# Kernel tuning notes

Hardware: AMD Instinct MI355X
Metric: run time of the kernel (lower is better)

## Reference

```python
import jax, jax.numpy as jnp
import numpy as np

B, T, N, F = 4, 24, 10000, 64
E = 160000
K_STEPS = 3
HID = 128


def setup_inputs() -> dict:
    key = jax.random.key(0)
    ks = jax.random.split(key, 12)
    history = jax.random.normal(ks[0], (B, T, N, F), dtype=jnp.float32)
    horizon = jax.random.normal(ks[1], (B, 6, N, F), dtype=jnp.float32)
    edge_index = jax.random.randint(ks[2], (2, E), 0, N, dtype=jnp.int64)
    s = 1.0 / np.sqrt(F)
    W_enc = jax.random.normal(ks[3], (F, F), dtype=jnp.float32) * s
    W_hor = jax.random.normal(ks[4], (F, F), dtype=jnp.float32) * s
    b_enc = jnp.zeros((F,), dtype=jnp.float32)
    W_fc = jax.random.normal(ks[5], (F, F), dtype=jnp.float32) * s  # EventGAN.fc (no bias)
    b_gcn = jax.random.normal(ks[6], (F,), dtype=jnp.float32) * 0.01  # EventGAN.bias
    W1 = jax.random.normal(ks[7], (T * F, HID), dtype=jnp.float32) / np.sqrt(T * F)
    b1 = jnp.zeros((HID,), dtype=jnp.float32)
    W2 = jax.random.normal(ks[8], (HID, 1), dtype=jnp.float32) / np.sqrt(HID)
    b2 = jnp.zeros((1,), dtype=jnp.float32)
    return {"history": history, "horizon": horizon, "edge_index": edge_index,
            "W_enc": W_enc, "W_hor": W_hor, "b_enc": b_enc,
            "W_fc": W_fc, "b_gcn": b_gcn,
            "W1": W1, "b1": b1, "W2": W2, "b2": b2}


def _event_gan_step(h, row, col, norm, W_fc, b_gcn, n_nodes):
    # h: [B, N, F]; GCN-style normalized sum aggregation (EventGAN.forward)
    x = h @ W_fc  # fc, no bias
    msgs = norm[None, :, None] * x[:, row, :]  # [B, Etot, F] gather + scale
    agg = jax.vmap(lambda m: jax.ops.segment_sum(m, col, num_segments=n_nodes))(msgs)
    return agg + b_gcn


def reference(history, horizon, edge_index, W_enc, W_hor, b_enc, W_fc, b_gcn, W1, b1, W2, b2):
    b, t, n, f = history.shape
    # FeatureEncoder (stand-in): per-timestep linear over F mixing pooled horizon context
    hor_ctx = jnp.mean(horizon, axis=1) @ W_hor  # [B, N, F]
    x = jnp.tanh(jnp.einsum('btnf,fg->btng', history, W_enc) + hor_ctx[:, None, :, :] + b_enc)
    # spatial: k-step EventGAN propagation on last timestep's exogenous features
    h = x[:, -1, :, -f:]  # [B, N, F] (F == exogenous_features)
    row0, col0 = edge_index[0], edge_index[1]
    loops = jnp.arange(n, dtype=edge_index.dtype)
    row = jnp.concatenate([row0, loops])
    col = jnp.concatenate([col0, loops])
    deg = jax.ops.segment_sum(jnp.ones_like(col, dtype=h.dtype), col, num_segments=n)
    dinv = jnp.where(deg > 0, jax.lax.rsqrt(jnp.maximum(deg, 1.0)), 0.0)
    norm = dinv[row] * dinv[col]
    for _ in range(K_STEPS):
        h = _event_gan_step(h, row, col, norm, W_fc, b_gcn, n)
    x = x.at[:, -1, :, -f:].set(h)
    # temporal MLP (stand-in): flatten per-node time series -> scalar
    flat = x.transpose(0, 2, 1, 3).reshape(b * n, t * f)
    out = jax.nn.relu(flat @ W1 + b1) @ W2 + b2  # [B*N, 1]
    return out.reshape(b, n)
```

## Files before the change

### kernel.cpp

```cpp
#include <hip/hip_runtime.h>

constexpr int cB = 4, cT = 24, cN = 10000, cF = 64, cE = 160000, cHID = 128, cK = 3;

typedef short s16x4 __attribute__((ext_vector_type(4)));
typedef short s16x8 __attribute__((ext_vector_type(8)));
typedef float f32x16 __attribute__((ext_vector_type(16)));

__device__ __forceinline__ unsigned short f2bf(float f) {
    union { float f; unsigned u; } c; c.f = f;
    unsigned u = c.u;
    return (unsigned short)((u + 0x7FFFu + ((u >> 16) & 1u)) >> 16);
}
__device__ __forceinline__ unsigned short f2bf_rtz(float f) {
    union { float f; unsigned u; } c; c.f = f;
    return (unsigned short)(c.u >> 16);
}
__device__ __forceinline__ unsigned asu(float f) {
    union { float f; unsigned u; } c; c.f = f; return c.u;
}

__device__ __forceinline__ float tanh_fast(float x) {
    float e = __expf(2.0f * x);
    return 1.0f - 2.0f * __builtin_amdgcn_rcpf(e + 1.0f);
}

__global__ void k_zeroA(int* __restrict__ cnt_in, int* __restrict__ cursor) {
    int i = blockIdx.x * 256 + threadIdx.x;
    if (i < cN) { cnt_in[i] = 0; cursor[i] = 0; }
}

__global__ void k_count(const int* __restrict__ edges, int* __restrict__ cnt_in) {
    int e = blockIdx.x * 256 + threadIdx.x;
    int nz = __syncthreads_count(e < cE && edges[2 * e + 1] == 0);
    if (e < cE) {
        int m = (nz == 256) ? 2 : 1;
        atomicAdd(&cnt_in[edges[m * (cE + e)]], 1);
    }
}

__global__ void k_scan(const int* __restrict__ cnt_in, int* __restrict__ rowptr,
                       float* __restrict__ dinv) {
    int lane = threadIdx.x;
    int carry = 0;
    for (int base = 0; base < cN; base += 1024) {
        int i0 = base + lane * 16;
        int v[16];
        int sum16 = 0;
        #pragma unroll
        for (int k = 0; k < 16; k++) {
            v[k] = (i0 + k < cN) ? cnt_in[i0 + k] : 0;
            sum16 += v[k];
        }
        int s = sum16;
        #pragma unroll
        for (int d = 1; d < 64; d <<= 1) {
            int u = __shfl_up(s, d, 64);
            if (lane >= d) s += u;
        }
        int pre = carry + s - sum16;
        #pragma unroll
        for (int k = 0; k < 16; k++) {
            if (i0 + k < cN) {
                rowptr[i0 + k] = pre;
                dinv[i0 + k] = rsqrtf((float)(v[k] + 1));
            }
            pre += v[k];
        }
        carry += __shfl(s, 63, 64);
    }
    if (lane == 0) rowptr[cN] = carry;
}

__global__ void k_fill(const int* __restrict__ edges, const int* __restrict__ rowptr,
                       int* __restrict__ cursor, int* __restrict__ csr_src) {
    int e = blockIdx.x * 256 + threadIdx.x;
    int nz = __syncthreads_count(e < cE && edges[2 * e + 1] == 0);
    if (e < cE) {
        int m = (nz == 256) ? 2 : 1;
        int r = edges[m * e];
        int c = edges[m * (cE + e)];
        int pos = atomicAdd(&cursor[c], 1);
        csr_src[rowptr[c] + pos] = r;
    }
}

__launch_bounds__(256)
__global__ void k_prep(const float* __restrict__ horizon, const float* __restrict__ W_hor,
                       const float* __restrict__ b_enc, float* __restrict__ hc,
                       const float* __restrict__ W1, unsigned short* __restrict__ W1T,
                       int hcB) {
    __shared__ float sLDS[64 * 65];
    __shared__ float sm[4][64];
    const int tid = threadIdx.x;
    if ((int)blockIdx.x < hcB) {
        float* sW = sLDS;
        {
            const float4* src = (const float4*)W_hor;
            float4* dst = (float4*)sW;
            #pragma unroll
            for (int q = 0; q < 4; q++) dst[tid + q * 256] = src[tid + q * 256];
        }
        int g = tid & 63;
        int sub = tid >> 6;
        int pair = blockIdx.x * 4 + sub;
        bool ok = pair < cB * cN;
        float m = 0.f;
        if (ok) {
            int b = pair / cN, n = pair % cN;
            const float* hp = horizon + ((size_t)(b * 6) * cN + n) * 64 + g;
            #pragma unroll
            for (int hh = 0; hh < 6; hh++) m += hp[(size_t)hh * cN * 64];
            m *= (1.0f / 6.0f);
        }
        sm[sub][g] = m;
        __syncthreads();
        if (!ok) return;
        float a = b_enc[g];
        #pragma unroll 8
        for (int f = 0; f < 64; f++) a = fmaf(sm[sub][f], sW[f * 64 + g], a);
        hc[(size_t)pair * 64 + g] = a;
    } else {
        float (*sT)[65] = (float(*)[65])sLDS;
        const int wb = blockIdx.x - hcB;
        const int t = wb % cT;
        const int hx = (wb / cT) * 64;
        const int gx = t * 64;
        #pragma unroll
        for (int r = 0; r < 4; r++) {
            int flat = tid + r * 256;
            int gp = flat >> 4, h4 = (flat & 15) * 4;
            float4 v = *(const float4*)&W1[(size_t)(gx + gp) * cHID + hx + h4];
            sT[h4 + 0][gp] = v.x; sT[h4 + 1][gp] = v.y;
            sT[h4 + 2][gp] = v.z; sT[h4 + 3][gp] = v.w;
        }
        __syncthreads();
        #pragma unroll
        for (int r = 0; r < 2; r++) {
            int flat = tid + r * 256;
            int h = flat >> 3, seg = flat & 7;
            s16x8 o;
            #pragma unroll
            for (int i = 0; i < 8; i++) o[i] = (short)f2bf(sT[h][seg * 8 + i]);
            *(s16x8*)&W1T[((size_t)t * cHID + hx + h) * 64 + seg * 8] = o;
        }
    }
}

__launch_bounds__(128, 2)
__global__ void k_encode_mlp(const float* __restrict__ history,
                             const float* __restrict__ W_enc,
                             const float* __restrict__ hc,
                             const unsigned short* __restrict__ W1T,
                             const float* __restrict__ dinv,
                             float* __restrict__ accbuf,
                             float* __restrict__ y0) {
    __shared__ unsigned short sHist[2][32 * 64];
    __shared__ unsigned short sXe[32 * 64];
    const int tid = threadIdx.x;
    const int lane = tid & 63;
    const int w = tid >> 6;
    const int l31 = lane & 31;
    const int lhi = lane >> 5;
    const int n0 = blockIdx.x * 32;
    const int b = blockIdx.y;
    const int zz = blockIdx.z;
    const int t0 = zz * (cT / 2), t1 = t0 + (cT / 2);
    const int nn = min(32, cN - n0);
    const int col = w * 32 + l31;

    float4 r[4];
    auto RLOAD = [&](int t) {
        const float* hsrc = history + ((size_t)(b * cT + t) * cN + n0) * 64;
        #pragma unroll
        for (int q = 0; q < 4; q++) {
            int flat = tid + q * 128;
            int node = flat >> 4, fq = flat & 15;
            r[q] = make_float4(0.f, 0.f, 0.f, 0.f);
            if (node < nn) r[q] = *(const float4*)(hsrc + node * 64 + fq * 4);
        }
    };
    auto SSTORE = [&](int buf) {
        #pragma unroll
        for (int q = 0; q < 4; q++) {
            int flat = tid + q * 128;
            int node = flat >> 4, fq = flat & 15;
            int2 p;
            p.x = (int)__builtin_amdgcn_perm(asu(r[q].y), asu(r[q].x), 0x07060302u);
            p.y = (int)__builtin_amdgcn_perm(asu(r[q].w), asu(r[q].z), 0x07060302u);
            int idx = (node * 64 + fq * 4) ^ ((node & 7) << 3);
            *(int2*)&sHist[buf][idx] = p;
        }
    };

    s16x8 wenc[4];
    #pragma unroll
    for (int ks = 0; ks < 4; ks++)
        #pragma unroll
        for (int i = 0; i < 8; i++)
            wenc[ks][i] = (short)f2bf(W_enc[(ks * 16 + lhi * 8 + i) * 64 + col]);

    float hcr[16];
    float dvr[16];
    #pragma unroll
    for (int reg = 0; reg < 16; reg++) {
        int row = (reg & 3) + 8 * (reg >> 2) + 4 * lhi;
        bool okr = row < nn;
        hcr[reg] = okr ? hc[(size_t)(b * cN + n0 + row) * 64 + col] : 0.f;
        dvr[reg] = okr ? dinv[n0 + row] : 0.f;
    }

    f32x16 accm[2];
    #pragma unroll
    for (int ht = 0; ht < 2; ht++)
        #pragma unroll
        for (int rr = 0; rr < 16; rr++) accm[ht][rr] = 0.f;

    RLOAD(t0);
    SSTORE(0);
    int cur = 0;

    for (int t = t0; t < t1; t++) {
        const bool last = (t == cT - 1);
        const bool have_next = (t + 1 < t1);
        if (have_next) RLOAD(t + 1);
        __syncthreads();
        f32x16 d;
        #pragma unroll
        for (int reg = 0; reg < 16; reg++) d[reg] = hcr[reg];
        {
            int base = l31 * 64 + lhi * 8;
            int sw = (l31 & 7) << 3;
            #pragma unroll
            for (int ks = 0; ks < 4; ks++) {
                s16x8 a = *(const s16x8*)&sHist[cur][(base + ks * 16) ^ sw];
                d = __builtin_amdgcn_mfma_f32_32x32x16_bf16(a, wenc[ks], d, 0, 0, 0);
            }
        }
        if (last) {
            #pragma unroll
            for (int reg = 0; reg < 16; reg++) {
                int row = (reg & 3) + 8 * (reg >> 2) + 4 * lhi;
                if (row < nn)
                    y0[(size_t)(n0 + row) * (cB * 64) + b * 64 + col] =
                        dvr[reg] * tanh_fast(d[reg]);
            }
        } else {
            #pragma unroll
            for (int reg = 0; reg < 16; reg++) {
                int row = (reg & 3) + 8 * (reg >> 2) + 4 * lhi;
                int idx = (row * 64 + col) ^ ((row & 7) << 3);
                sXe[idx] = f2bf_rtz(tanh_fast(d[reg]));
            }
            __syncthreads();
            int bbase = l31 * 64 + lhi * 8;
            int swB = (l31 & 7) << 3;
            #pragma unroll
            for (int ht = 0; ht < 2; ht++) {
                const unsigned short* wrow =
                    W1T + ((size_t)t * cHID + (w * 64 + ht * 32 + l31)) * 64 + lhi * 8;
                #pragma unroll
                for (int ks = 0; ks < 4; ks++) {
                    s16x8 aw = *(const s16x8*)(wrow + ks * 16);
                    s16x8 bx = *(const s16x8*)&sXe[(bbase + ks * 16) ^ swB];
                    accm[ht] = __builtin_amdgcn_mfma_f32_32x32x16_bf16(aw, bx, accm[ht], 0, 0, 0);
                }
            }
        }
        if (have_next) SSTORE(cur ^ 1);
        cur ^= 1;
    }
    int node = l31;
    if (node < nn) {
        float* ap = accbuf + (size_t)zz * cB * cN * cHID + (size_t)(b * cN + n0 + node) * cHID;
        #pragma unroll
        for (int ht = 0; ht < 2; ht++) {
            #pragma unroll
            for (int q = 0; q < 4; q++) {
                int hid0 = w * 64 + ht * 32 + q * 8 + lhi * 4;
                float4 v = make_float4(accm[ht][q * 4 + 0], accm[ht][q * 4 + 1],
                                       accm[ht][q * 4 + 2], accm[ht][q * 4 + 3]);
                *(float4*)(ap + hid0) = v;
            }
        }
    }
}

__launch_bounds__(512)
__global__ void k_gstep(const int* __restrict__ rowptr, const int* __restrict__ csr_src,
                        const float* __restrict__ dinv, const float* __restrict__ yin,
                        const float* __restrict__ W_fc, const float* __restrict__ b_gcn,
                        float* __restrict__ yout) {
    __shared__ float sW[64 * 64];
    __shared__ float sAgg[4][4][64];
    const int tid = threadIdx.x;
    {
        const float4* src = (const float4*)W_fc;
        float4* dst = (float4*)sW;
        #pragma unroll
        for (int q = 0; q < 2; q++) dst[tid + q * 512] = src[tid + q * 512];
    }
    const int wv = tid >> 6;
    const int nl = wv >> 1;
    const int bp = wv & 1;
    const int g = tid & 63;
    const int n = blockIdx.x * 4 + nl;
    if (n < cN) {
        const float* yn = yin + (size_t)n * 256 + bp * 128;
        float a0 = yn[g], a1 = yn[64 + g];
        int i = rowptr[n], end = rowptr[n + 1];
        for (; i + 4 <= end; i += 4) {
            int s0 = csr_src[i + 0], s1 = csr_src[i + 1];
            int s2 = csr_src[i + 2], s3 = csr_src[i + 3];
            const float* x0 = yin + (size_t)s0 * 256 + bp * 128;
            const float* x1 = yin + (size_t)s1 * 256 + bp * 128;
            const float* x2 = yin + (size_t)s2 * 256 + bp * 128;
            const float* x3 = yin + (size_t)s3 * 256 + bp * 128;
            float v00 = x0[g], v01 = x0[64 + g];
            float v10 = x1[g], v11 = x1[64 + g];
            float v20 = x2[g], v21 = x2[64 + g];
            float v30 = x3[g], v31 = x3[64 + g];
            a0 += (v00 + v10) + (v20 + v30);
            a1 += (v01 + v11) + (v21 + v31);
        }
        for (; i < end; i++) {
            int s = csr_src[i];
            const float* xs = yin + (size_t)s * 256 + bp * 128;
            a0 += xs[g]; a1 += xs[64 + g];
        }
        sAgg[nl][bp * 2 + 0][g] = a0;
        sAgg[nl][bp * 2 + 1][g] = a1;
    }
    __syncthreads();
    if (n >= cN) return;
    const float* g0 = sAgg[nl][bp * 2 + 0];
    const float* g1 = sAgg[nl][bp * 2 + 1];
    float o0 = 0.f, o1 = 0.f;
    #pragma unroll 8
    for (int f = 0; f < 64; f++) {
        float wv_ = sW[f * 64 + g];
        o0 = fmaf(g0[f], wv_, o0);
        o1 = fmaf(g1[f], wv_, o1);
    }
    float di = dinv[n], bg = b_gcn[g];
    float h0v = fmaf(di, o0, bg) * di;
    float h1v = fmaf(di, o1, bg) * di;
    yout[(size_t)n * 256 + (bp * 2 + 0) * 64 + g] = h0v;
    yout[(size_t)n * 256 + (bp * 2 + 1) * 64 + g] = h1v;
}

__launch_bounds__(512)
__global__ void k_gstep_head(const int* __restrict__ rowptr, const int* __restrict__ csr_src,
                             const float* __restrict__ dinv, const float* __restrict__ yin,
                             const float* __restrict__ W_fc, const float* __restrict__ b_gcn,
                             const float* __restrict__ accbuf,
                             const float* __restrict__ W1, const float* __restrict__ b1,
                             const float* __restrict__ W2, const float* __restrict__ b2,
                             float* __restrict__ out) {
    __shared__ float sW[64 * 64];
    __shared__ float sAgg[4][4][64];
    const int tid = threadIdx.x;
    {
        const float4* src = (const float4*)W_fc;
        float4* dst = (float4*)sW;
        #pragma unroll
        for (int q = 0; q < 2; q++) dst[tid + q * 512] = src[tid + q * 512];
    }
    const int wv = tid >> 6;
    const int nl = wv >> 1;
    const int bp = wv & 1;
    const int g = tid & 63;
    const int n = blockIdx.x * 4 + nl;
    if (n < cN) {
        const float* yn = yin + (size_t)n * 256 + bp * 128;
        float a0 = yn[g], a1 = yn[64 + g];
        int i = rowptr[n], end = rowptr[n + 1];
        for (; i + 4 <= end; i += 4) {
            int s0 = csr_src[i + 0], s1 = csr_src[i + 1];
            int s2 = csr_src[i + 2], s3 = csr_src[i + 3];
            const float* x0 = yin + (size_t)s0 * 256 + bp * 128;
            const float* x1 = yin + (size_t)s1 * 256 + bp * 128;
            const float* x2 = yin + (size_t)s2 * 256 + bp * 128;
            const float* x3 = yin + (size_t)s3 * 256 + bp * 128;
            float v00 = x0[g], v01 = x0[64 + g];
            float v10 = x1[g], v11 = x1[64 + g];
            float v20 = x2[g], v21 = x2[64 + g];
            float v30 = x3[g], v31 = x3[64 + g];
            a0 += (v00 + v10) + (v20 + v30);
            a1 += (v01 + v11) + (v21 + v31);
        }
        for (; i < end; i++) {
            int s = csr_src[i];
            const float* xs = yin + (size_t)s * 256 + bp * 128;
            a0 += xs[g]; a1 += xs[64 + g];
        }
        sAgg[nl][bp * 2 + 0][g] = a0;
        sAgg[nl][bp * 2 + 1][g] = a1;
    }
    __syncthreads();
    float h0v = 0.f, h1v = 0.f;
    if (n < cN) {
        const float* g0 = sAgg[nl][bp * 2 + 0];
        const float* g1 = sAgg[nl][bp * 2 + 1];
        float o0 = 0.f, o1 = 0.f;
        #pragma unroll 8
        for (int f = 0; f < 64; f++) {
            float wv_ = sW[f * 64 + g];
            o0 = fmaf(g0[f], wv_, o0);
            o1 = fmaf(g1[f], wv_, o1);
        }
        float di = dinv[n], bg = b_gcn[g];
        h0v = fmaf(di, o0, bg);
        h1v = fmaf(di, o1, bg);
    }
    __syncthreads();
    if (n < cN) {
        sAgg[nl][bp * 2 + 0][g] = h0v;
        sAgg[nl][bp * 2 + 1][g] = h1v;
    }
    __syncthreads();
    if (n >= cN) return;
    const float* w1p = W1 + (size_t)(cT - 1) * 64 * cHID;
    float b1a = b1[g], b1b = b1[g + 64];
    float w2a = W2[g], w2b = W2[g + 64];
    #pragma unroll
    for (int pi = 0; pi < 2; pi++) {
        int bb = bp * 2 + pi;
        size_t pair = (size_t)bb * cN + n;
        const float* hrow = sAgg[nl][bb];
        const float* ac0 = accbuf + pair * cHID;
        const float* ac1 = accbuf + (size_t)cB * cN * cHID + pair * cHID;
        float a0 = ac0[g] + ac1[g] + b1a;
        float a1 = ac0[g + 64] + ac1[g + 64] + b1b;
        #pragma unroll 8
        for (int f = 0; f < 64; f++) {
            float hv = hrow[f];
            a0 = fmaf(hv, w1p[f * cHID + g], a0);
            a1 = fmaf(hv, w1p[f * cHID + g + 64], a1);
        }
        float s = fmaxf(a0, 0.f) * w2a + fmaxf(a1, 0.f) * w2b;
        #pragma unroll
        for (int d2 = 32; d2 > 0; d2 >>= 1) s += __shfl_down(s, d2, 64);
        if (g == 0) out[pair] = s + b2[0];
    }
}

extern "C" void kernel_launch(void* const* d_in, const int* in_sizes, int n_in,
                              void* d_out, int out_size, void* d_ws, size_t ws_size,
                              hipStream_t stream) {
    const float* history = (const float*)d_in[0];
    const float* horizon = (const float*)d_in[1];
    const int*   edges   = (const int*)d_in[2];
    const float* W_enc   = (const float*)d_in[3];
    const float* W_hor   = (const float*)d_in[4];
    const float* b_enc   = (const float*)d_in[5];
    const float* W_fc    = (const float*)d_in[6];
    const float* b_gcn   = (const float*)d_in[7];
    const float* W1      = (const float*)d_in[8];
    const float* b1      = (const float*)d_in[9];
    const float* W2      = (const float*)d_in[10];
    const float* b2      = (const float*)d_in[11];
    float* out = (float*)d_out;

    float* ws = (float*)d_ws;
    float* hc     = ws;
    float* accbuf = hc + (size_t)cB * cN * 64;
    float* yA     = accbuf + (size_t)2 * cB * cN * cHID;
    float* yB     = yA + (size_t)cB * cN * 64;
    float* dinv   = yB + (size_t)cB * cN * 64;
    unsigned short* w1t = (unsigned short*)(dinv + cN);
    int*   cnt_in = (int*)(w1t + (size_t)cT * cHID * 64);
    int*   cursor = cnt_in + cN;
    int*   rowptr = cursor + cN;
    int*   csr_src= rowptr + cN + 1;

    const int hcB = (cB * cN + 3) / 4;

    k_zeroA<<<(cN + 255) / 256, 256, 0, stream>>>(cnt_in, cursor);
    k_count<<<(cE + 255) / 256, 256, 0, stream>>>(edges, cnt_in);
    k_scan<<<1, 64, 0, stream>>>(cnt_in, rowptr, dinv);
    k_fill<<<(cE + 255) / 256, 256, 0, stream>>>(edges, rowptr, cursor, csr_src);

    k_prep<<<hcB + cT * 2, 256, 0, stream>>>(horizon, W_hor, b_enc, hc, W1, w1t, hcB);
    k_encode_mlp<<<dim3((cN + 31) / 32, cB, 2), 128, 0, stream>>>(history, W_enc, hc,
                                                                  w1t, dinv, accbuf, yA);

    k_gstep<<<(cN + 3) / 4, 512, 0, stream>>>(rowptr, csr_src, dinv, yA, W_fc, b_gcn, yB);
    k_gstep<<<(cN + 3) / 4, 512, 0, stream>>>(rowptr, csr_src, dinv, yB, W_fc, b_gcn, yA);
    k_gstep_head<<<(cN + 3) / 4, 512, 0, stream>>>(rowptr, csr_src, dinv, yA, W_fc, b_gcn,
                                                   accbuf, W1, b1, W2, b2, out);
}
```

Measured before the change: 315.6 us.

## Split encoder time range four ways and unroll gather loop by eight

The encode+MLP kernel now splits the 24 timesteps into four z-slices instead of two. That doubles grid parallelism, but it writes four partial accumulator buffers, which the head kernel then sums. The graph-step gather loops gain an 8-wide unrolled path so more independent neighbor loads are in flight at once. The cost is more accumulator memory traffic and workspace, plus possible redundant per-block setup in the encoder.

```diff
diff --git a/kernel.cpp b/kernel.cpp
--- a/kernel.cpp
+++ b/kernel.cpp
@@ -1,6 +1,7 @@
 #include <hip/hip_runtime.h>
 
 constexpr int cB = 4, cT = 24, cN = 10000, cF = 64, cE = 160000, cHID = 128, cK = 3;
+constexpr int cZ = 4;
 
 typedef short s16x4 __attribute__((ext_vector_type(4)));
 typedef short s16x8 __attribute__((ext_vector_type(8)));
@@ -164,7 +165,7 @@
     const int n0 = blockIdx.x * 32;
     const int b = blockIdx.y;
     const int zz = blockIdx.z;
-    const int t0 = zz * (cT / 2), t1 = t0 + (cT / 2);
+    const int t0 = zz * (cT / cZ), t1 = t0 + (cT / cZ);
     const int nn = min(32, cN - n0);
     const int col = w * 32 + l31;
 
@@ -308,6 +309,18 @@
         const float* yn = yin + (size_t)n * 256 + bp * 128;
         float a0 = yn[g], a1 = yn[64 + g];
         int i = rowptr[n], end = rowptr[n + 1];
+        for (; i + 8 <= end; i += 8) {
+            int s[8];
+            #pragma unroll
+            for (int k = 0; k < 8; k++) s[k] = csr_src[i + k];
+            float t0 = 0.f, t1 = 0.f;
+            #pragma unroll
+            for (int k = 0; k < 8; k++) {
+                const float* xs = yin + (size_t)s[k] * 256 + bp * 128;
+                t0 += xs[g]; t1 += xs[64 + g];
+            }
+            a0 += t0; a1 += t1;
+        }
         for (; i + 4 <= end; i += 4) {
             int s0 = csr_src[i + 0], s1 = csr_src[i + 1];
             int s2 = csr_src[i + 2], s3 = csr_src[i + 3];
@@ -315,12 +328,8 @@
             const float* x1 = yin + (size_t)s1 * 256 + bp * 128;
             const float* x2 = yin + (size_t)s2 * 256 + bp * 128;
             const float* x3 = yin + (size_t)s3 * 256 + bp * 128;
-            float v00 = x0[g], v01 = x0[64 + g];
-            float v10 = x1[g], v11 = x1[64 + g];
-            float v20 = x2[g], v21 = x2[64 + g];
-            float v30 = x3[g], v31 = x3[64 + g];
-            a0 += (v00 + v10) + (v20 + v30);
-            a1 += (v01 + v11) + (v21 + v31);
+            a0 += (x0[g] + x1[g]) + (x2[g] + x3[g]);
+            a1 += (x0[64 + g] + x1[64 + g]) + (x2[64 + g] + x3[64 + g]);
         }
         for (; i < end; i++) {
             int s = csr_src[i];
@@ -374,6 +383,18 @@
         const float* yn = yin + (size_t)n * 256 + bp * 128;
         float a0 = yn[g], a1 = yn[64 + g];
         int i = rowptr[n], end = rowptr[n + 1];
+        for (; i + 8 <= end; i += 8) {
+            int s[8];
+            #pragma unroll
+            for (int k = 0; k < 8; k++) s[k] = csr_src[i + k];
+            float t0 = 0.f, t1 = 0.f;
+            #pragma unroll
+            for (int k = 0; k < 8; k++) {
+                const float* xs = yin + (size_t)s[k] * 256 + bp * 128;
+                t0 += xs[g]; t1 += xs[64 + g];
+            }
+            a0 += t0; a1 += t1;
+        }
         for (; i + 4 <= end; i += 4) {
             int s0 = csr_src[i + 0], s1 = csr_src[i + 1];
             int s2 = csr_src[i + 2], s3 = csr_src[i + 3];
@@ -381,12 +402,8 @@
             const float* x1 = yin + (size_t)s1 * 256 + bp * 128;
             const float* x2 = yin + (size_t)s2 * 256 + bp * 128;
             const float* x3 = yin + (size_t)s3 * 256 + bp * 128;
-            float v00 = x0[g], v01 = x0[64 + g];
-            float v10 = x1[g], v11 = x1[64 + g];
-            float v20 = x2[g], v21 = x2[64 + g];
-            float v30 = x3[g], v31 = x3[64 + g];
-            a0 += (v00 + v10) + (v20 + v30);
-            a1 += (v01 + v11) + (v21 + v31);
+            a0 += (x0[g] + x1[g]) + (x2[g] + x3[g]);
+            a1 += (x0[64 + g] + x1[64 + g]) + (x2[64 + g] + x3[64 + g]);
         }
         for (; i < end; i++) {
             int s = csr_src[i];
@@ -427,10 +444,13 @@
         int bb = bp * 2 + pi;
         size_t pair = (size_t)bb * cN + n;
         const float* hrow = sAgg[nl][bb];
-        const float* ac0 = accbuf + pair * cHID;
-        const float* ac1 = accbuf + (size_t)cB * cN * cHID + pair * cHID;
-        float a0 = ac0[g] + ac1[g] + b1a;
-        float a1 = ac0[g + 64] + ac1[g + 64] + b1b;
+        float a0 = b1a, a1 = b1b;
+        #pragma unroll
+        for (int z = 0; z < cZ; z++) {
+            const float* ac = accbuf + (size_t)z * cB * cN * cHID + pair * cHID;
+            a0 += ac[g];
+            a1 += ac[g + 64];
+        }
         #pragma unroll 8
         for (int f = 0; f < 64; f++) {
             float hv = hrow[f];
@@ -464,7 +484,7 @@
     float* ws = (float*)d_ws;
     float* hc     = ws;
     float* accbuf = hc + (size_t)cB * cN * 64;
-    float* yA     = accbuf + (size_t)2 * cB * cN * cHID;
+    float* yA     = accbuf + (size_t)cZ * cB * cN * cHID;
     float* yB     = yA + (size_t)cB * cN * 64;
     float* dinv   = yB + (size_t)cB * cN * 64;
     unsigned short* w1t = (unsigned short*)(dinv + cN);
@@ -481,8 +501,8 @@
     k_fill<<<(cE + 255) / 256, 256, 0, stream>>>(edges, rowptr, cursor, csr_src);
 
     k_prep<<<hcB + cT * 2, 256, 0, stream>>>(horizon, W_hor, b_enc, hc, W1, w1t, hcB);
-    k_encode_mlp<<<dim3((cN + 31) / 32, cB, 2), 128, 0, stream>>>(history, W_enc, hc,
-                                                                  w1t, dinv, accbuf, yA);
+    k_encode_mlp<<<dim3((cN + 31) / 32, cB, cZ), 128, 0, stream>>>(history, W_enc, hc,
+                                                                   w1t, dinv, accbuf, yA);
 
     k_gstep<<<(cN + 3) / 4, 512, 0, stream>>>(rowptr, csr_src, dinv, yA, W_fc, b_gcn, yB);
     k_gstep<<<(cN + 3) / 4, 512, 0, stream>>>(rowptr, csr_src, dinv, yB, W_fc, b_gcn, yA);
```

New measurement: 316.7 us. About the same (+0.3%).
